# Performance work log

Measured on AMD Instinct MI355X. Metric: run time of the kernel, lower is better.

## Reference

```python
import jax, jax.numpy as jnp
import numpy as np

N_USER = 100_000
N_ITEM = 50_000
C = 128
E = 600_000
L = 2          # num_layers
NN = 2         # num_layers_nn (MLP depth inside GINConv)
LN_EPS = 1e-5


def _layernorm(x, g, b):
    # PyG LayerNorm(mode='node'): normalize each node over channels, affine
    m = jnp.mean(x, axis=-1, keepdims=True)
    v = jnp.mean((x - m) ** 2, axis=-1, keepdims=True)
    return (x - m) * jax.lax.rsqrt(v + LN_EPS) * g + b


def _mlp(x, W, b):
    # GINConv inner MLP: [Linear -> ReLU] * NN
    for i in range(NN):
        x = jax.nn.relu(x @ W[i] + b[i])
    return x


def setup_inputs() -> dict:
    key = jax.random.key(0)
    ks = jax.random.split(key, 10)
    s = 1.0 / np.sqrt(C)
    edge_ui = jnp.stack([
        jax.random.randint(ks[0], (E,), 0, N_USER, dtype=jnp.int32),  # src: user
        jax.random.randint(ks[1], (E,), 0, N_ITEM, dtype=jnp.int32),  # dst: item
    ])
    edge_iu = jnp.stack([
        jax.random.randint(ks[2], (E,), 0, N_ITEM, dtype=jnp.int32),  # src: item
        jax.random.randint(ks[3], (E,), 0, N_USER, dtype=jnp.int32),  # dst: user
    ])
    return {
        "x_user": jax.random.normal(ks[4], (N_USER, C), dtype=jnp.float32),
        "x_item": jax.random.normal(ks[5], (N_ITEM, C), dtype=jnp.float32),
        "W_init": jax.random.normal(ks[6], (2, C, C), dtype=jnp.float32) * s,
        "b_init": jnp.zeros((2, C), dtype=jnp.float32),
        "mlp_W": jax.random.normal(ks[7], (L, 2, NN, C, C), dtype=jnp.float32) * s,
        "mlp_b": jnp.zeros((L, 2, NN, C), dtype=jnp.float32),
        "eps": jnp.full((L, 2), 1e-5, dtype=jnp.float32),  # train_eps=True, init eps=1e-5
        "ln_g": jnp.ones((L, 2, C), dtype=jnp.float32),
        "ln_b": jnp.zeros((L, 2, C), dtype=jnp.float32),
        "edge_ui": edge_ui,
        "edge_iu": edge_iu,
    }


def reference(x_user, x_item, W_init, b_init, mlp_W, mlp_b, eps, ln_g, ln_b,
              edge_ui, edge_iu):
    # Initial per-node-type projection (LazyLinear)
    xu = x_user @ W_init[0] + b_init[0]
    xi = x_item @ W_init[1] + b_init[1]
    for l in range(L):
        # GINConv per edge type; HeteroConv(aggr='sum') trivially reduces since
        # each node type is targeted by exactly one edge type here.
        agg_i = jax.ops.segment_sum(xu[edge_ui[0]], edge_ui[1], num_segments=N_ITEM)
        agg_u = jax.ops.segment_sum(xi[edge_iu[0]], edge_iu[1], num_segments=N_USER)
        # edge_type index 0 = (user->item), 1 = (item->user)
        new_i = _mlp((1.0 + eps[l, 0]) * xi + agg_i, mlp_W[l, 0], mlp_b[l, 0])
        new_u = _mlp((1.0 + eps[l, 1]) * xu + agg_u, mlp_W[l, 1], mlp_b[l, 1])
        # node_type index 0 = user, 1 = item
        xu = jax.nn.relu(_layernorm(new_u, ln_g[l, 0], ln_b[l, 0]))
        xi = jax.nn.relu(_layernorm(new_i, ln_g[l, 1], ln_b[l, 1]))
    return (xu, xi)
```

## Files before the change

kernel.cpp:

```cpp
#include <hip/hip_runtime.h>
#include <cstdint>
#include <cstddef>

#define N_USER 100000
#define N_ITEM 50000
#define CDIM   128
#define NEDGE  600000
#define N_SEG  (N_ITEM + N_USER)
#define NB_SCAN ((N_SEG + 255) / 256)

#define FILL_EPB 2048
#define FILL_NCHUNK ((NEDGE + FILL_EPB - 1) / FILL_EPB)
#define SLICE_DIV ((N_SEG + 7) / 8)

typedef __bf16 bf16_t;
typedef bf16_t bfvec8 __attribute__((ext_vector_type(8)));
typedef bf16_t bfvec4 __attribute__((ext_vector_type(4)));
typedef float  f32x4  __attribute__((ext_vector_type(4)));

#define LDW 136

__global__ __launch_bounds__(256) void prep_weights(
    const float* __restrict__ W_init, const float* __restrict__ mlp_W,
    bf16_t* __restrict__ wtg)
{
    int m  = blockIdx.x >> 6;
    int it = blockIdx.x & 63;
    const float* src = (m < 2) ? (W_init + (size_t)m * 16384)
                               : (mlp_W + (size_t)(m - 2) * 16384);
    int e = it * 256 + threadIdx.x;
    int n = e >> 7, k = e & 127;
    wtg[(size_t)m * 16384 + e] = (bf16_t)src[k * 128 + n];
}

template <int NT>
static __device__ inline void stage_wbf(bf16_t* Wt, const bf16_t* __restrict__ Wg, int tid) {
    #pragma unroll
    for (int c = tid; c < 2048; c += NT) {
        int n = c >> 4, koff = (c & 15) * 8;
        *reinterpret_cast<bfvec8*>(&Wt[n * LDW + koff]) =
            *reinterpret_cast<const bfvec8*>(&Wg[n * 128 + koff]);
    }
}

__global__ __launch_bounds__(512) void gemm_init(
    const float* __restrict__ X,
    const bf16_t* __restrict__ Wg,
    const float* __restrict__ B,
    bf16_t* __restrict__ Y, int M)
{
    __shared__ __align__(16) bf16_t Wt[128 * LDW];
    const int tid = threadIdx.x;
    stage_wbf<512>(Wt, Wg, tid);
    __syncthreads();

    const int wave = tid >> 6, lane = tid & 63;
    const int quad = lane >> 4, ln16 = lane & 15;
    const int row_l = wave * 16 + ln16;
    const int rowg = blockIdx.x * 128 + row_l;
    const int rowc = rowg < M ? rowg : 0;

    bfvec8 xb[4];
    const float* xp = X + (size_t)rowc * CDIM + quad * 8;
    #pragma unroll
    for (int kc = 0; kc < 4; ++kc) {
        f32x4 lo = *reinterpret_cast<const f32x4*>(xp + kc * 32);
        f32x4 hi = *reinterpret_cast<const f32x4*>(xp + kc * 32 + 4);
        #pragma unroll
        for (int j = 0; j < 4; ++j) {
            xb[kc][j]     = (bf16_t)lo[j];
            xb[kc][j + 4] = (bf16_t)hi[j];
        }
    }

    f32x4 acc[8];
    #pragma unroll
    for (int t = 0; t < 8; ++t) acc[t] = (f32x4){0.f, 0.f, 0.f, 0.f};
    #pragma unroll
    for (int t = 0; t < 8; ++t) {
        const bf16_t* wp = &Wt[(t * 16 + ln16) * LDW + quad * 8];
        #pragma unroll
        for (int kc = 0; kc < 4; ++kc) {
            bfvec8 wv = *reinterpret_cast<const bfvec8*>(wp + kc * 32);
            acc[t] = __builtin_amdgcn_mfma_f32_16x16x32_bf16(wv, xb[kc], acc[t], 0, 0, 0);
        }
    }

    if (rowg < M) {
        #pragma unroll
        for (int t = 0; t < 8; ++t) {
            f32x4 bv = *reinterpret_cast<const f32x4*>(&B[t * 16 + quad * 4]);
            bfvec4 o;
            #pragma unroll
            for (int r = 0; r < 4; ++r) o[r] = (bf16_t)(acc[t][r] + bv[r]);
            *reinterpret_cast<bfvec4*>(&Y[(size_t)rowg * CDIM + t * 16 + quad * 4]) = o;
        }
    }
}

__global__ __launch_bounds__(256) void zero_i32(int* __restrict__ p, int n)
{
    int i = blockIdx.x * 256 + threadIdx.x;
    if (i < n) p[i] = 0;
}

__global__ __launch_bounds__(256) void hist_rank(
    const int* __restrict__ edge_ui, const int* __restrict__ edge_iu,
    int* __restrict__ deg, int2* __restrict__ rank2)
{
    int i = blockIdx.x * 256 + threadIdx.x;
    if (i >= NEDGE) return;
    int r0 = atomicAdd(&deg[edge_ui[NEDGE + i]], 1);
    int r1 = atomicAdd(&deg[N_ITEM + edge_iu[NEDGE + i]], 1);
    rank2[i] = make_int2(r0, r1);
}

__global__ __launch_bounds__(256) void block_scan(
    int* __restrict__ off, int* __restrict__ bsum, int n)
{
    __shared__ int sh[256];
    int tid = threadIdx.x;
    int i = blockIdx.x * 256 + tid;
    int v = (i < n) ? off[i] : 0;
    sh[tid] = v;
    __syncthreads();
    #pragma unroll
    for (int d = 1; d < 256; d <<= 1) {
        int t = (tid >= d) ? sh[tid - d] : 0;
        __syncthreads();
        sh[tid] += t;
        __syncthreads();
    }
    if (i < n) off[i] = sh[tid] - v;
    if (tid == 255) bsum[blockIdx.x] = sh[255];
}

__global__ __launch_bounds__(1024) void scan_bsums(int* __restrict__ bsum)
{
    __shared__ int sh[1024];
    int tid = threadIdx.x;
    int v = (tid < NB_SCAN) ? bsum[tid] : 0;
    sh[tid] = v;
    __syncthreads();
    #pragma unroll
    for (int d = 1; d < 1024; d <<= 1) {
        int t = (tid >= d) ? sh[tid - d] : 0;
        __syncthreads();
        sh[tid] += t;
        __syncthreads();
    }
    if (tid < NB_SCAN) bsum[tid] = sh[tid] - v;
    if (tid == 1023) bsum[NB_SCAN] = sh[1023];
}

__global__ __launch_bounds__(256) void add_offsets(
    int* __restrict__ off, const int* __restrict__ bsum, int n)
{
    int i = blockIdx.x * 256 + threadIdx.x;
    if (i < n) off[i] += bsum[i >> 8];
    else if (i == n) off[n] = bsum[NB_SCAN];
}

__global__ __launch_bounds__(256) void fill_sliced(
    const int* __restrict__ edge_ui, const int* __restrict__ edge_iu,
    const int* __restrict__ off, const int2* __restrict__ rank2,
    int* __restrict__ srcbuf)
{
    const int r = blockIdx.x & 7;
    const int chunk = blockIdx.x >> 3;
    const int base = chunk * FILL_EPB + threadIdx.x;
    #pragma unroll
    for (int j = 0; j < FILL_EPB / 256; ++j) {
        int i = base + j * 256;
        if (i < NEDGE) {
            int d0 = edge_ui[NEDGE + i];
            int d1 = edge_iu[NEDGE + i] + N_ITEM;
            int2 rk = rank2[i];
            if (d0 / SLICE_DIV == r)
                srcbuf[off[d0] + rk.x] = edge_ui[i];
            if (d1 / SLICE_DIV == r)
                srcbuf[off[d1] + rk.y] = edge_iu[i];
        }
    }
}

__global__ __launch_bounds__(256) void gather_both(
    const bf16_t* __restrict__ xu, const bf16_t* __restrict__ xi,
    const float* __restrict__ eps2,
    const int* __restrict__ off_all, const int* __restrict__ srcbuf,
    bf16_t* __restrict__ ti, bf16_t* __restrict__ tu)
{
    const int gBI = (N_ITEM + 3) / 4;
    int b = blockIdx.x;
    bool isItem = b < gBI;
    int wave = threadIdx.x >> 6;
    int node = (isItem ? b : b - gBI) * 4 + wave;
    int n = isItem ? N_ITEM : N_USER;
    if (node >= n) return;

    const bfvec8* F = reinterpret_cast<const bfvec8*>(isItem ? xu : xi);
    const bfvec8* X = reinterpret_cast<const bfvec8*>(isItem ? xi : xu);
    const int* off = isItem ? off_all : off_all + N_ITEM;
    bfvec8* out = reinterpret_cast<bfvec8*>(isItem ? ti : tu);
    float s = 1.f + (isItem ? eps2[0] : eps2[1]);

    int lane = threadIdx.x & 63;
    int grp  = lane >> 4;
    int l16  = lane & 15;
    int start = off[node], end = off[node + 1];

    float acc[8];
    #pragma unroll
    for (int j = 0; j < 8; ++j) acc[j] = 0.f;

    int e = start + grp;
    for (; e + 12 < end; e += 16) {
        int s0 = srcbuf[e];
        int s1 = srcbuf[e + 4];
        int s2 = srcbuf[e + 8];
        int s3 = srcbuf[e + 12];
        bfvec8 v0 = F[(size_t)s0 * 16 + l16];
        bfvec8 v1 = F[(size_t)s1 * 16 + l16];
        bfvec8 v2 = F[(size_t)s2 * 16 + l16];
        bfvec8 v3 = F[(size_t)s3 * 16 + l16];
        #pragma unroll
        for (int j = 0; j < 8; ++j)
            acc[j] += ((float)v0[j] + (float)v1[j]) + ((float)v2[j] + (float)v3[j]);
    }
    for (; e + 4 < end; e += 8) {
        int s0 = srcbuf[e];
        int s1 = srcbuf[e + 4];
        bfvec8 v0 = F[(size_t)s0 * 16 + l16];
        bfvec8 v1 = F[(size_t)s1 * 16 + l16];
        #pragma unroll
        for (int j = 0; j < 8; ++j) acc[j] += (float)v0[j] + (float)v1[j];
    }
    for (; e < end; e += 4) {
        bfvec8 v = F[(size_t)srcbuf[e] * 16 + l16];
        #pragma unroll
        for (int j = 0; j < 8; ++j) acc[j] += (float)v[j];
    }

    #pragma unroll
    for (int j = 0; j < 8; ++j) {
        acc[j] += __shfl_xor(acc[j], 16, 64);
        acc[j] += __shfl_xor(acc[j], 32, 64);
    }

    if (grp == 0) {
        bfvec8 xv = X[(size_t)node * 16 + l16];
        bfvec8 o;
        #pragma unroll
        for (int j = 0; j < 8; ++j) o[j] = (bf16_t)(s * (float)xv[j] + acc[j]);
        out[(size_t)node * 16 + l16] = o;
    }
}

__global__ __launch_bounds__(512) void mlp_ln_both(
    const bf16_t* __restrict__ ti, const bf16_t* __restrict__ tu,
    const bf16_t* __restrict__ wg,
    const float* __restrict__ mlpb,
    const float* __restrict__ lng,
    const float* __restrict__ lnb,
    bf16_t* __restrict__ xib, bf16_t* __restrict__ xub,
    float* __restrict__ xif, float* __restrict__ xuf,
    int f32out)
{
    __shared__ __align__(16) bf16_t Wt[128 * LDW];
    __shared__ __align__(16) bf16_t At[128 * LDW];

    const int gBI = (N_ITEM + 127) / 128;
    int b = blockIdx.x;
    bool isItem = b < gBI;
    const bf16_t* X = isItem ? ti : tu;
    bf16_t* Yb      = isItem ? xib : xub;
    float*  Yf      = isItem ? xif : xuf;
    int M  = isItem ? N_ITEM : N_USER;
    int bx = isItem ? b : b - gBI;
    const bf16_t* W1 = wg + (isItem ? 0 : 2) * 16384;
    const bf16_t* W2 = W1 + 16384;
    const float* B1 = mlpb + (isItem ? 0 : 2) * 128;
    const float* B2 = B1 + 128;
    const float* G  = lng + (isItem ? 128 : 0);
    const float* Bb = lnb + (isItem ? 128 : 0);

    const int tid = threadIdx.x;
    stage_wbf<512>(Wt, W1, tid);
    __syncthreads();

    const int wave = tid >> 6, lane = tid & 63;
    const int quad = lane >> 4, ln16 = lane & 15;
    const int row_l = wave * 16 + ln16;
    const int rowg = bx * 128 + row_l;
    const int rowc = rowg < M ? rowg : 0;

    bfvec8 xb[4];
    const bf16_t* xp = X + (size_t)rowc * CDIM + quad * 8;
    #pragma unroll
    for (int kc = 0; kc < 4; ++kc)
        xb[kc] = *reinterpret_cast<const bfvec8*>(xp + kc * 32);

    f32x4 acc[8];
    #pragma unroll
    for (int t = 0; t < 8; ++t) acc[t] = (f32x4){0.f, 0.f, 0.f, 0.f};
    #pragma unroll
    for (int t = 0; t < 8; ++t) {
        const bf16_t* wp = &Wt[(t * 16 + ln16) * LDW + quad * 8];
        #pragma unroll
        for (int kc = 0; kc < 4; ++kc) {
            bfvec8 wv = *reinterpret_cast<const bfvec8*>(wp + kc * 32);
            acc[t] = __builtin_amdgcn_mfma_f32_16x16x32_bf16(wv, xb[kc], acc[t], 0, 0, 0);
        }
    }

    #pragma unroll
    for (int t = 0; t < 8; ++t) {
        f32x4 bv = *reinterpret_cast<const f32x4*>(&B1[t * 16 + quad * 4]);
        bfvec4 o;
        #pragma unroll
        for (int r = 0; r < 4; ++r) {
            float v = acc[t][r] + bv[r];
            o[r] = (bf16_t)(v > 0.f ? v : 0.f);
        }
        *reinterpret_cast<bfvec4*>(&At[row_l * LDW + t * 16 + quad * 4]) = o;
    }
    __syncthreads();
    stage_wbf<512>(Wt, W2, tid);
    __syncthreads();

    bfvec8 hb[4];
    #pragma unroll
    for (int kc = 0; kc < 4; ++kc)
        hb[kc] = *reinterpret_cast<const bfvec8*>(&At[row_l * LDW + kc * 32 + quad * 8]);

    #pragma unroll
    for (int t = 0; t < 8; ++t) acc[t] = (f32x4){0.f, 0.f, 0.f, 0.f};
    #pragma unroll
    for (int t = 0; t < 8; ++t) {
        const bf16_t* wp = &Wt[(t * 16 + ln16) * LDW + quad * 8];
        #pragma unroll
        for (int kc = 0; kc < 4; ++kc) {
            bfvec8 wv = *reinterpret_cast<const bfvec8*>(wp + kc * 32);
            acc[t] = __builtin_amdgcn_mfma_f32_16x16x32_bf16(wv, hb[kc], acc[t], 0, 0, 0);
        }
    }

    #pragma unroll
    for (int t = 0; t < 8; ++t) {
        f32x4 bv = *reinterpret_cast<const f32x4*>(&B2[t * 16 + quad * 4]);
        #pragma unroll
        for (int r = 0; r < 4; ++r) {
            float v = acc[t][r] + bv[r];
            acc[t][r] = v > 0.f ? v : 0.f;
        }
    }

    float sm = 0.f;
    #pragma unroll
    for (int t = 0; t < 8; ++t)
        #pragma unroll
        for (int r = 0; r < 4; ++r) sm += acc[t][r];
    sm += __shfl_xor(sm, 16, 64);
    sm += __shfl_xor(sm, 32, 64);
    float mean = sm * (1.f / 128.f);
    float sq = 0.f;
    #pragma unroll
    for (int t = 0; t < 8; ++t)
        #pragma unroll
        for (int r = 0; r < 4; ++r) { float d = acc[t][r] - mean; sq += d * d; }
    sq += __shfl_xor(sq, 16, 64);
    sq += __shfl_xor(sq, 32, 64);
    float rs = rsqrtf(sq * (1.f / 128.f) + 1e-5f);

    if (rowg < M) {
        if (f32out) {
            #pragma unroll
            for (int t = 0; t < 8; ++t) {
                f32x4 g4 = *reinterpret_cast<const f32x4*>(&G[t * 16 + quad * 4]);
                f32x4 b4 = *reinterpret_cast<const f32x4*>(&Bb[t * 16 + quad * 4]);
                f32x4 y;
                #pragma unroll
                for (int r = 0; r < 4; ++r) {
                    float v = (acc[t][r] - mean) * rs * g4[r] + b4[r];
                    y[r] = v > 0.f ? v : 0.f;
                }
                *reinterpret_cast<f32x4*>(&Yf[(size_t)rowg * CDIM + t * 16 + quad * 4]) = y;
            }
        } else {
            #pragma unroll
            for (int t = 0; t < 8; ++t) {
                f32x4 g4 = *reinterpret_cast<const f32x4*>(&G[t * 16 + quad * 4]);
                f32x4 b4 = *reinterpret_cast<const f32x4*>(&Bb[t * 16 + quad * 4]);
                bfvec4 y;
                #pragma unroll
                for (int r = 0; r < 4; ++r) {
                    float v = (acc[t][r] - mean) * rs * g4[r] + b4[r];
                    y[r] = (bf16_t)(v > 0.f ? v : 0.f);
                }
                *reinterpret_cast<bfvec4*>(&Yb[(size_t)rowg * CDIM + t * 16 + quad * 4]) = y;
            }
        }
    }
}

extern "C" void kernel_launch(void* const* d_in, const int* in_sizes, int n_in,
                              void* d_out, int out_size, void* d_ws, size_t ws_size,
                              hipStream_t stream)
{
    const float* x_user = (const float*)d_in[0];
    const float* x_item = (const float*)d_in[1];
    const float* W_init = (const float*)d_in[2];
    const float* b_init = (const float*)d_in[3];
    const float* mlp_W  = (const float*)d_in[4];
    const float* mlp_b  = (const float*)d_in[5];
    const float* eps    = (const float*)d_in[6];
    const float* ln_g   = (const float*)d_in[7];
    const float* ln_b   = (const float*)d_in[8];
    const int* edge_ui  = (const int*)d_in[9];
    const int* edge_iu  = (const int*)d_in[10];

    float* xuf = (float*)d_out;
    float* xif = xuf + (size_t)N_USER * CDIM;

    char* w = (char*)d_ws;
    bf16_t* xub = (bf16_t*)w;
    bf16_t* xib = xub + (size_t)N_USER * CDIM;
    bf16_t* tub = xib + (size_t)N_ITEM * CDIM;
    bf16_t* tib = tub + (size_t)N_USER * CDIM;
    int* off_all = (int*)(tib + (size_t)N_ITEM * CDIM);
    int* bsum    = off_all + (N_SEG + 4);
    int* srcbuf  = bsum + (NB_SCAN + 2);
    bf16_t* wtg  = (bf16_t*)(srcbuf + 2 * NEDGE);

    int2* rank2 = (int2*)tub;

    const int gU = (N_USER + 127) / 128;
    const int gI = (N_ITEM + 127) / 128;
    const int gSeg = (N_SEG + 256) / 256;
    const int gE = (NEDGE + 255) / 256;
    const int gGather = (N_ITEM + 3) / 4 + (N_USER + 3) / 4;

    prep_weights<<<640, 256, 0, stream>>>(W_init, mlp_W, wtg);

    zero_i32<<<(N_SEG + 255) / 256, 256, 0, stream>>>(off_all, N_SEG);
    hist_rank<<<gE, 256, 0, stream>>>(edge_ui, edge_iu, off_all, rank2);
    block_scan<<<NB_SCAN, 256, 0, stream>>>(off_all, bsum, N_SEG);
    scan_bsums<<<1, 1024, 0, stream>>>(bsum);
    add_offsets<<<gSeg, 256, 0, stream>>>(off_all, bsum, N_SEG);
    fill_sliced<<<FILL_NCHUNK * 8, 256, 0, stream>>>(edge_ui, edge_iu, off_all, rank2, srcbuf);

    gemm_init<<<gU, 512, 0, stream>>>(x_user, wtg,         b_init,       xub, N_USER);
    gemm_init<<<gI, 512, 0, stream>>>(x_item, wtg + 16384, b_init + 128, xib, N_ITEM);

    for (int l = 0; l < 2; ++l) {
        gather_both<<<gGather, 256, 0, stream>>>(
            xub, xib, eps + 2 * l, off_all, srcbuf, tib, tub);
        mlp_ln_both<<<gI + gU, 512, 0, stream>>>(
            tib, tub, wtg + (size_t)(2 + l * 4) * 16384, mlp_b + l * 4 * 128,
            ln_g + l * 2 * 128, ln_b + l * 2 * 128,
            xib, xub, xif, xuf, (l == 1) ? 1 : 0);
    }
}
```

Before: 467.7 us.

## Slice CSR histogram and fill by destination range, drop rank buffer, reuse LDS

Result: slower. 498.1 us (+6.5%).

```diff
diff --git a/kernel.cpp b/kernel.cpp
--- a/kernel.cpp
+++ b/kernel.cpp
@@ -9,9 +9,10 @@
 #define N_SEG  (N_ITEM + N_USER)
 #define NB_SCAN ((N_SEG + 255) / 256)
 
-#define FILL_EPB 2048
-#define FILL_NCHUNK ((NEDGE + FILL_EPB - 1) / FILL_EPB)
-#define SLICE_DIV ((N_SEG + 7) / 8)
+#define EPB 2048
+#define NCHUNK ((NEDGE + EPB - 1) / EPB)
+#define ISL 12500
+#define USL 25000
 
 typedef __bf16 bf16_t;
 typedef bf16_t bfvec8 __attribute__((ext_vector_type(8)));
@@ -104,15 +105,33 @@
     if (i < n) p[i] = 0;
 }
 
-__global__ __launch_bounds__(256) void hist_rank(
+__global__ __launch_bounds__(256) void hist_sliced(
     const int* __restrict__ edge_ui, const int* __restrict__ edge_iu,
-    int* __restrict__ deg, int2* __restrict__ rank2)
-{
-    int i = blockIdx.x * 256 + threadIdx.x;
-    if (i >= NEDGE) return;
-    int r0 = atomicAdd(&deg[edge_ui[NEDGE + i]], 1);
-    int r1 = atomicAdd(&deg[N_ITEM + edge_iu[NEDGE + i]], 1);
-    rank2[i] = make_int2(r0, r1);
+    int* __restrict__ deg)
+{
+    const int r = blockIdx.x & 7;
+    const int base = (blockIdx.x >> 3) * EPB + threadIdx.x;
+    if (r < 4) {
+        const int lo = r * ISL, hi = lo + ISL;
+        #pragma unroll
+        for (int j = 0; j < EPB / 256; ++j) {
+            int i = base + j * 256;
+            if (i < NEDGE) {
+                int d = edge_ui[NEDGE + i];
+                if (d >= lo && d < hi) atomicAdd(&deg[d], 1);
+            }
+        }
+    } else {
+        const int lo = (r - 4) * USL, hi = lo + USL;
+        #pragma unroll
+        for (int j = 0; j < EPB / 256; ++j) {
+            int i = base + j * 256;
+            if (i < NEDGE) {
+                int d = edge_iu[NEDGE + i];
+                if (d >= lo && d < hi) atomicAdd(&deg[N_ITEM + d], 1);
+            }
+        }
+    }
 }
 
 __global__ __launch_bounds__(256) void block_scan(
@@ -154,32 +173,50 @@
 }
 
 __global__ __launch_bounds__(256) void add_offsets(
-    int* __restrict__ off, const int* __restrict__ bsum, int n)
+    int* __restrict__ off, const int* __restrict__ bsum,
+    int* __restrict__ cursor, int n)
 {
     int i = blockIdx.x * 256 + threadIdx.x;
-    if (i < n) off[i] += bsum[i >> 8];
-    else if (i == n) off[n] = bsum[NB_SCAN];
-}
-
-__global__ __launch_bounds__(256) void fill_sliced(
+    if (i < n) {
+        int o = off[i] + bsum[i >> 8];
+        off[i] = o;
+        cursor[i] = o;
+    } else if (i == n) {
+        off[n] = bsum[NB_SCAN];
+    }
+}
+
+__global__ __launch_bounds__(256) void fill_csr(
     const int* __restrict__ edge_ui, const int* __restrict__ edge_iu,
-    const int* __restrict__ off, const int2* __restrict__ rank2,
-    int* __restrict__ srcbuf)
+    int* __restrict__ cursor, int* __restrict__ srcbuf)
 {
     const int r = blockIdx.x & 7;
-    const int chunk = blockIdx.x >> 3;
-    const int base = chunk * FILL_EPB + threadIdx.x;
-    #pragma unroll
-    for (int j = 0; j < FILL_EPB / 256; ++j) {
-        int i = base + j * 256;
-        if (i < NEDGE) {
-            int d0 = edge_ui[NEDGE + i];
-            int d1 = edge_iu[NEDGE + i] + N_ITEM;
-            int2 rk = rank2[i];
-            if (d0 / SLICE_DIV == r)
-                srcbuf[off[d0] + rk.x] = edge_ui[i];
-            if (d1 / SLICE_DIV == r)
-                srcbuf[off[d1] + rk.y] = edge_iu[i];
+    const int base = (blockIdx.x >> 3) * EPB + threadIdx.x;
+    if (r < 4) {
+        const int lo = r * ISL, hi = lo + ISL;
+        #pragma unroll
+        for (int j = 0; j < EPB / 256; ++j) {
+            int i = base + j * 256;
+            if (i < NEDGE) {
+                int d = edge_ui[NEDGE + i];
+                if (d >= lo && d < hi) {
+                    int slot = atomicAdd(&cursor[d], 1);
+                    srcbuf[slot] = edge_ui[i];
+                }
+            }
+        }
+    } else {
+        const int lo = (r - 4) * USL, hi = lo + USL;
+        #pragma unroll
+        for (int j = 0; j < EPB / 256; ++j) {
+            int i = base + j * 256;
+            if (i < NEDGE) {
+                int d = edge_iu[NEDGE + i];
+                if (d >= lo && d < hi) {
+                    int slot = atomicAdd(&cursor[N_ITEM + d], 1);
+                    srcbuf[slot] = edge_iu[i];
+                }
+            }
         }
     }
 }
@@ -256,7 +293,7 @@
     }
 }
 
-__global__ __launch_bounds__(512) void mlp_ln_both(
+__global__ __launch_bounds__(512, 6) void mlp_ln_both(
     const bf16_t* __restrict__ ti, const bf16_t* __restrict__ tu,
     const bf16_t* __restrict__ wg,
     const float* __restrict__ mlpb,
@@ -267,7 +304,6 @@
     int f32out)
 {
     __shared__ __align__(16) bf16_t Wt[128 * LDW];
-    __shared__ __align__(16) bf16_t At[128 * LDW];
 
     const int gBI = (N_ITEM + 127) / 128;
     int b = blockIdx.x;
@@ -312,6 +348,7 @@
             acc[t] = __builtin_amdgcn_mfma_f32_16x16x32_bf16(wv, xb[kc], acc[t], 0, 0, 0);
         }
     }
+    __syncthreads();
 
     #pragma unroll
     for (int t = 0; t < 8; ++t) {
@@ -322,16 +359,18 @@
             float v = acc[t][r] + bv[r];
             o[r] = (bf16_t)(v > 0.f ? v : 0.f);
         }
-        *reinterpret_cast<bfvec4*>(&At[row_l * LDW + t * 16 + quad * 4]) = o;
-    }
-    __syncthreads();
+        *reinterpret_cast<bfvec4*>(&Wt[row_l * LDW + t * 16 + quad * 4]) = o;
+    }
+    __syncthreads();
+
+    bfvec8 hb[4];
+    #pragma unroll
+    for (int kc = 0; kc < 4; ++kc)
+        hb[kc] = *reinterpret_cast<const bfvec8*>(&Wt[row_l * LDW + kc * 32 + quad * 8]);
+    __syncthreads();
+
     stage_wbf<512>(Wt, W2, tid);
     __syncthreads();
-
-    bfvec8 hb[4];
-    #pragma unroll
-    for (int kc = 0; kc < 4; ++kc)
-        hb[kc] = *reinterpret_cast<const bfvec8*>(&At[row_l * LDW + kc * 32 + quad * 8]);
 
     #pragma unroll
     for (int t = 0; t < 8; ++t) acc[t] = (f32x4){0.f, 0.f, 0.f, 0.f};
@@ -428,26 +467,24 @@
     bf16_t* tub = xib + (size_t)N_ITEM * CDIM;
     bf16_t* tib = tub + (size_t)N_USER * CDIM;
     int* off_all = (int*)(tib + (size_t)N_ITEM * CDIM);
-    int* bsum    = off_all + (N_SEG + 4);
+    int* cursor  = off_all + (N_SEG + 4);
+    int* bsum    = cursor + N_SEG;
     int* srcbuf  = bsum + (NB_SCAN + 2);
     bf16_t* wtg  = (bf16_t*)(srcbuf + 2 * NEDGE);
-
-    int2* rank2 = (int2*)tub;
 
     const int gU = (N_USER + 127) / 128;
     const int gI = (N_ITEM + 127) / 128;
     const int gSeg = (N_SEG + 256) / 256;
-    const int gE = (NEDGE + 255) / 256;
     const int gGather = (N_ITEM + 3) / 4 + (N_USER + 3) / 4;
 
     prep_weights<<<640, 256, 0, stream>>>(W_init, mlp_W, wtg);
 
     zero_i32<<<(N_SEG + 255) / 256, 256, 0, stream>>>(off_all, N_SEG);
-    hist_rank<<<gE, 256, 0, stream>>>(edge_ui, edge_iu, off_all, rank2);
+    hist_sliced<<<NCHUNK * 8, 256, 0, stream>>>(edge_ui, edge_iu, off_all);
     block_scan<<<NB_SCAN, 256, 0, stream>>>(off_all, bsum, N_SEG);
     scan_bsums<<<1, 1024, 0, stream>>>(bsum);
-    add_offsets<<<gSeg, 256, 0, stream>>>(off_all, bsum, N_SEG);
-    fill_sliced<<<FILL_NCHUNK * 8, 256, 0, stream>>>(edge_ui, edge_iu, off_all, rank2, srcbuf);
+    add_offsets<<<gSeg, 256, 0, stream>>>(off_all, bsum, cursor, N_SEG);
+    fill_csr<<<NCHUNK * 8, 256, 0, stream>>>(edge_ui, edge_iu, cursor, srcbuf);
 
     gemm_init<<<gU, 512, 0, stream>>>(x_user, wtg,         b_init,       xub, N_USER);
     gemm_init<<<gI, 512, 0, stream>>>(x_item, wtg + 16384, b_init + 128, xib, N_ITEM);
```
